# Optimization experiments

Measured on AMD Instinct MI355X. Metric: run time of the kernel, lower is better.

The kernel has to match this reference:

```python
import jax, jax.numpy as jnp
import numpy as np

B, N = 32, 512            # batch, max nodes per graph
F_DIM, M_DIM = 1024, 256  # node feature dim, first hidden dim
N_SEM = 8                 # number of semantic-class experts
XYZ, DIM_E = 3, 8
OUT_SIZE = 2 * XYZ + DIM_E  # 14 (default reg branch)
EPS = 1e-8                # padding value used by out_seq_to_batch


def setup_inputs() -> dict:
    key = jax.random.key(0)
    ks = jax.random.split(key, 12)
    def w(k, shape, fan_in):
        return jax.random.normal(k, shape, jnp.float32) / np.float32(np.sqrt(fan_in))
    return {
        "nodes": jax.random.normal(ks[0], (B, N, F_DIM), jnp.float32),
        "sem": jax.random.randint(ks[1], (B, N), 0, N_SEM, jnp.int32),
        "lengths": jax.random.randint(ks[2], (B,), 64, N + 1, jnp.int32),
        # y expert MLPs (4 layers), stacked over experts
        "W1": w(ks[3], (N_SEM, F_DIM, M_DIM), F_DIM), "b1": jnp.zeros((N_SEM, M_DIM), jnp.float32),
        "W2": w(ks[4], (N_SEM, M_DIM, 64), M_DIM),   "b2": jnp.zeros((N_SEM, 64), jnp.float32),
        "W3": w(ks[5], (N_SEM, 64, 32), 64),         "b3": jnp.zeros((N_SEM, 32), jnp.float32),
        "W4": w(ks[6], (N_SEM, 32, OUT_SIZE), 32),   "b4": jnp.zeros((N_SEM, OUT_SIZE), jnp.float32),
        # rot expert MLPs (2 layers), stacked over experts
        "R1": w(ks[7], (N_SEM, F_DIM, M_DIM), F_DIM), "rb1": jnp.zeros((N_SEM, M_DIM), jnp.float32),
        "R2": w(ks[8], (N_SEM, M_DIM, XYZ), M_DIM),   "rb2": jnp.zeros((N_SEM, XYZ), jnp.float32),
    }


def _prim_mlps(nodes, sem, lengths, W1, b1, W2, b2, W3, b3, W4, b4, R1, rb1, R2, rb2):
    Bn, Nn, Fd = nodes.shape
    x = nodes.reshape(-1, Fd)                       # [T, F], T = B*N tokens
    semf = sem.reshape(-1)                          # [T] expert id per token
    # dense dispatch: run every expert on all tokens, then select per token
    h1 = jax.nn.relu(jnp.einsum('tf,efm->etm', x, W1) + b1[:, None, :])   # [E,T,M]
    h2 = jax.nn.relu(jnp.einsum('etm,emh->eth', h1, W2) + b2[:, None, :]) # [E,T,64]
    h3 = jax.nn.relu(jnp.einsum('eth,ehg->etg', h2, W3) + b3[:, None, :]) # [E,T,32]
    y_all = jnp.einsum('etg,ego->eto', h3, W4) + b4[:, None, :]           # [E,T,OUT]
    r1 = jax.nn.relu(jnp.einsum('tf,efm->etm', x, R1) + rb1[:, None, :])  # [E,T,M]
    rot_all = jnp.einsum('etm,emo->eto', r1, R2) + rb2[:, None, :]        # [E,T,XYZ]
    t = jnp.arange(x.shape[0])
    y = y_all[semf, t]                              # [T, OUT]
    rot = rot_all[semf, t]                          # [T, XYZ]
    out = jnp.concatenate([y, rot], axis=-1).reshape(Bn, Nn, -1)
    # positions beyond each graph's length are filled with eps (out_seq_to_batch)
    mask = (jnp.arange(Nn)[None, :] < lengths[:, None])[:, :, None]
    return jnp.where(mask, out, jnp.float32(EPS))


def reference(nodes, sem, lengths, W1, b1, W2, b2, W3, b3, W4, b4, R1, rb1, R2, rb2):
    return _prim_mlps(nodes, sem, lengths, W1, b1, W2, b2, W3, b3, W4, b4,
                      R1, rb1, R2, rb2)
```

## Files before the change

### kernel.cpp

```cpp
#include <hip/hip_runtime.h>
#include <stdint.h>

#define T_TOK 16384
#define NE 8
#define EPSV 1e-8f
#define MAXC128 136
#define MAXC64  264

#define WS_PERM   0
#define WS_PART   65536
#define WS_OFFS   67584
#define WS_XS     131072
#define WS_WT     (WS_XS + 16512*1024*2)
#define WS_H1     (WS_WT + 8*512*1024*2)
#define WS_W2T    (WS_H1 + 16448*512*2)
#define WS_W3T    (WS_W2T + 8*64*256*2)
#define WS_W4T    (WS_W3T + 8*32*64*2)
#define WS_R2T    (WS_W4T + 8*16*32*2)

typedef __attribute__((ext_vector_type(8))) short bf16x8;
typedef __attribute__((ext_vector_type(4))) float f32x4;

__device__ __forceinline__ unsigned short f2bf(float f) {
    unsigned u = __float_as_uint(f);
    u += 0x7fffu + ((u >> 16) & 1u);
    return (unsigned short)(u >> 16);
}

__device__ __forceinline__ void gl_lds16(const void* g, void* l) {
    __builtin_amdgcn_global_load_lds(
        (const __attribute__((address_space(1))) void*)g,
        (__attribute__((address_space(3))) void*)l,
        16, 0, 0);
}

__device__ __forceinline__ bool chunk_lookup(const int* __restrict__ offs, int c, int csize,
                                             int& e, int& base, int& len) {
    int acc = 0;
#pragma unroll
    for (int i = 0; i < NE; i++) {
        int s = offs[i], t = offs[i + 1];
        int cc = (t - s + csize - 1) / csize;
        if (c < acc + cc) {
            e = i;
            base = s + (c - acc) * csize;
            len = (t - base < csize) ? (t - base) : csize;
            return true;
        }
        acc += cc;
    }
    return false;
}

__global__ __launch_bounds__(256) void k_prep1(const float* __restrict__ W1,
                                               const float* __restrict__ R1,
                                               const float* __restrict__ W2,
                                               const float* __restrict__ W3,
                                               const float* __restrict__ W4,
                                               const float* __restrict__ R2,
                                               const int* __restrict__ sem,
                                               unsigned short* __restrict__ wt,
                                               unsigned short* __restrict__ w2t,
                                               unsigned short* __restrict__ w3t,
                                               unsigned short* __restrict__ w4t,
                                               unsigned short* __restrict__ r2t,
                                               int* __restrict__ ws_i) {
    __shared__ float tile[64][65];
    int id = blockIdx.x, tid = threadIdx.x;
    if (id >= 1024) {
        __shared__ int cnt[NE];
        int hb = id - 1024, lane = tid & 63;
        if (tid < NE) cnt[tid] = 0;
        __syncthreads();
        int s = sem[hb * 256 + tid];
#pragma unroll
        for (int e = 0; e < NE; e++) {
            unsigned long long m = __ballot(s == e);
            if (lane == e) atomicAdd(&cnt[e], (int)__popcll(m));
        }
        __syncthreads();
        if (tid < NE) ws_i[(WS_PART >> 2) + hb * NE + tid] = cnt[tid];
        return;
    }
    int e = id >> 7, rem = id & 127;
    int ny = rem >> 4, kx = rem & 15;
    int k0 = kx * 64, n0 = ny * 64;
    const float* src = (n0 < 256) ? (W1 + (size_t)e * 1024 * 256 + n0)
                                  : (R1 + (size_t)e * 1024 * 256 + (n0 - 256));
    int rr = tid >> 4;
    int cg = (tid & 15) * 4;
#pragma unroll
    for (int p = 0; p < 4; p++) {
        int kk = p * 16 + rr;
        float4 v = *(const float4*)(src + (size_t)(k0 + kk) * 256 + cg);
        tile[kk][cg] = v.x; tile[kk][cg + 1] = v.y; tile[kk][cg + 2] = v.z; tile[kk][cg + 3] = v.w;
    }
    __syncthreads();
    int nn = tid >> 3;
    int k8 = tid & 7;
#pragma unroll
    for (int p = 0; p < 2; p++) {
        int n = p * 32 + nn;
        unsigned w[4];
#pragma unroll
        for (int j = 0; j < 4; j++) {
            float f0 = tile[k8 * 8 + 2 * j][n];
            float f1 = tile[k8 * 8 + 2 * j + 1][n];
            w[j] = (unsigned)f2bf(f0) | ((unsigned)f2bf(f1) << 16);
        }
        *(uint4*)(wt + (size_t)(e * 512 + n0 + n) * 1024 + k0 + k8 * 8) =
            make_uint4(w[0], w[1], w[2], w[3]);
    }
    if (ny == 0) {
        int x = kx;
        for (int j = tid; j < 1024; j += 256) {
            int idx = x * 1024 + j; int k = idx & 255, n = idx >> 8;
            w2t[(size_t)(e * 64 + n) * 256 + k] = f2bf(W2[(size_t)e * 16384 + k * 64 + n]);
        }
        if (tid < 128) {
            int idx = x * 128 + tid; int k = idx & 63, n = idx >> 6;
            w3t[(size_t)(e * 32 + n) * 64 + k] = f2bf(W3[(size_t)e * 2048 + k * 32 + n]);
        }
        if (tid < 32) {
            int idx = x * 32 + tid; int k = idx & 31, n = idx >> 5;
            w4t[(size_t)(e * 16 + n) * 32 + k] = (n < 14) ? f2bf(W4[(size_t)e * 448 + k * 14 + n])
                                                          : (unsigned short)0;
        }
        {
            int idx = x * 256 + tid; int k = idx & 255, n = idx >> 8;
            r2t[(size_t)(e * 16 + n) * 256 + k] = (n < 3) ? f2bf(R2[(size_t)e * 768 + k * 3 + n])
                                                          : (unsigned short)0;
        }
    }
}

__global__ __launch_bounds__(256) void k_scatter(const int* __restrict__ sem,
                                                 const float* __restrict__ nodes,
                                                 int* __restrict__ ws_i,
                                                 unsigned short* __restrict__ xs) {
    __shared__ int parts[512];
    __shared__ int tot[NE], preb[NE], ebase[NE + 1];
    __shared__ int wcnt[4][NE];
    __shared__ int destS[256];
    int b = blockIdx.x, g = b >> 3, j = b & 7;
    int tid = threadIdx.x, wave = tid >> 6, lane = tid & 63;
    parts[tid] = ws_i[(WS_PART >> 2) + tid];
    parts[256 + tid] = ws_i[(WS_PART >> 2) + 256 + tid];
    __syncthreads();
    if (tid < NE) {
        int t = 0, p = 0;
        for (int bb = 0; bb < 64; bb++) {
            int v = parts[bb * NE + tid];
            t += v;
            if (bb < g) p += v;
        }
        tot[tid] = t; preb[tid] = p;
    }
    __syncthreads();
    if (tid == 0) {
        int base = 0;
        for (int e = 0; e < NE; e++) { ebase[e] = base; base += tot[e]; }
        ebase[NE] = base;
        if (b == 0)
            for (int e = 0; e <= NE; e++) ws_i[(WS_OFFS >> 2) + e] = ebase[e];
    }
    int i = g * 256 + tid;
    int s = sem[i];
    int rank = 0;
#pragma unroll
    for (int e = 0; e < NE; e++) {
        unsigned long long m = __ballot(s == e);
        if (s == e) rank = (int)__popcll(m & ((1ull << lane) - 1ull));
        if (lane == e) wcnt[wave][e] = (int)__popcll(m);
    }
    __syncthreads();
    int wpre = 0;
#pragma unroll
    for (int w = 0; w < 4; w++)
        if (w < wave) wpre += wcnt[w][s];
    int dest = ebase[s] + preb[s] + wpre + rank;
    destS[tid] = dest;
    if (j == 0) ws_i[(WS_PERM >> 2) + dest] = i;
    __syncthreads();
#pragma unroll 4
    for (int r = j * 32; r < j * 32 + 32; r++) {
        int tok = g * 256 + r;
        int d = destS[r];
        float4 v = *(const float4*)(nodes + (size_t)tok * 1024 + tid * 4);
        unsigned p0 = (unsigned)f2bf(v.x) | ((unsigned)f2bf(v.y) << 16);
        unsigned p1 = (unsigned)f2bf(v.z) | ((unsigned)f2bf(v.w) << 16);
        *(uint2*)(xs + (size_t)d * 1024 + tid * 4) = make_uint2(p0, p1);
    }
}

__global__ __launch_bounds__(256) void k_gemm(const unsigned short* __restrict__ xs,
                                              const unsigned short* __restrict__ wt,
                                              const float* __restrict__ b1,
                                              const float* __restrict__ rb1,
                                              const int* __restrict__ ws_i,
                                              unsigned short* __restrict__ h1) {
    __shared__ __align__(16) short As[64 * 64];
    __shared__ __align__(16) short Bs[128 * 64];
    int e, base, len;
    if (!chunk_lookup(ws_i + (WS_OFFS >> 2), blockIdx.x, 64, e, base, len)) return;
    int n0 = blockIdx.y * 128;
    int tid = threadIdx.x;
    int wave = tid >> 6, lane = tid & 63;
    int quad = lane >> 4, lr = lane & 15;
    int wn = wave * 32;

    f32x4 acc[4][2];
#pragma unroll
    for (int i = 0; i < 4; i++)
#pragma unroll
        for (int j = 0; j < 2; j++) acc[i][j] = (f32x4){0.f, 0.f, 0.f, 0.f};

    const unsigned short* Ag = xs + (size_t)base * 1024;
    const unsigned short* Bg = wt + (size_t)(e * 512 + n0) * 1024;

    const unsigned short* srcA[2];
    int dstA[2];
#pragma unroll
    for (int i = 0; i < 2; i++) {
        int s = i * 256 + wave * 64 + lane;
        int r = s >> 3, cs = (s & 7) ^ (r & 7);
        srcA[i] = Ag + (size_t)r * 1024 + cs * 8;
        dstA[i] = (i * 256 + wave * 64) * 8;
    }
    const unsigned short* srcB[4];
    int dstB[4];
#pragma unroll
    for (int i = 0; i < 4; i++) {
        int s = i * 256 + wave * 64 + lane;
        int r = s >> 3, cs = (s & 7) ^ (r & 7);
        srcB[i] = Bg + (size_t)r * 1024 + cs * 8;
        dstB[i] = (i * 256 + wave * 64) * 8;
    }

    for (int kb = 0; kb < 16; kb++) {
        __syncthreads();
#pragma unroll
        for (int i = 0; i < 2; i++) gl_lds16(srcA[i] + kb * 64, As + dstA[i]);
#pragma unroll
        for (int i = 0; i < 4; i++) gl_lds16(srcB[i] + kb * 64, Bs + dstB[i]);
        __syncthreads();

        bf16x8 af[2][4], bfr[2][2];
#pragma unroll
        for (int im = 0; im < 4; im++) {
            int r = im * 16 + lr;
#pragma unroll
            for (int kh = 0; kh < 2; kh++) {
                int q = kh * 4 + quad;
                af[kh][im] = *(const bf16x8*)(As + (r * 8 + (q ^ (r & 7))) * 8);
            }
        }
#pragma unroll
        for (int in = 0; in < 2; in++) {
            int r = wn + in * 16 + lr;
#pragma unroll
            for (int kh = 0; kh < 2; kh++) {
                int q = kh * 4 + quad;
                bfr[kh][in] = *(const bf16x8*)(Bs + (r * 8 + (q ^ (r & 7))) * 8);
            }
        }
#pragma unroll
        for (int kh = 0; kh < 2; kh++)
#pragma unroll
            for (int im = 0; im < 4; im++)
#pragma unroll
                for (int in = 0; in < 2; in++)
                    acc[im][in] = __builtin_amdgcn_mfma_f32_16x16x32_bf16(af[kh][im], bfr[kh][in], acc[im][in], 0, 0, 0);
    }

#pragma unroll
    for (int in = 0; in < 2; in++) {
        int gcol = n0 + wn + in * 16 + lr;
        float bias = (gcol < 256) ? b1[e * 256 + gcol] : rb1[e * 256 + gcol - 256];
#pragma unroll
        for (int im = 0; im < 4; im++) {
#pragma unroll
            for (int v = 0; v < 4; v++) {
                int r = im * 16 + quad * 4 + v;
                if (r < len) {
                    float val = fmaxf(acc[im][in][v] + bias, 0.f);
                    h1[(size_t)(base + r) * 512 + gcol] = f2bf(val);
                }
            }
        }
    }
}

__global__ __launch_bounds__(256) void k_tail(const unsigned short* __restrict__ h1,
                                              const int* __restrict__ ws_i,
                                              const unsigned short* __restrict__ w2t,
                                              const unsigned short* __restrict__ w3t,
                                              const unsigned short* __restrict__ w4t,
                                              const unsigned short* __restrict__ r2t,
                                              const float* __restrict__ b2,
                                              const float* __restrict__ b3,
                                              const float* __restrict__ b4,
                                              const float* __restrict__ rb2,
                                              const int* __restrict__ lengths,
                                              float* __restrict__ out) {
    __shared__ __align__(16) unsigned short h2s[4][16][64];
    __shared__ __align__(16) unsigned short h3s[4][16][32];

    int e, base, len;
    if (!chunk_lookup(ws_i + (WS_OFFS >> 2), blockIdx.x, 64, e, base, len)) return;
    int tid = threadIdx.x, wave = tid >> 6, lane = tid & 63;
    int quad = lane >> 4, lr = lane & 15;
    int m0 = wave * 16;

    const unsigned short* Ap = h1 + (size_t)(base + m0) * 512;

    f32x4 acc2[4];
#pragma unroll
    for (int t = 0; t < 4; t++) {
        float bb = b2[e * 64 + t * 16 + lr];
        acc2[t] = (f32x4){bb, bb, bb, bb};
    }
    f32x4 accr;
    { float bb = (lr < 3) ? rb2[e * 3 + lr] : 0.f; accr = (f32x4){bb, bb, bb, bb}; }

    const unsigned short* W2e = w2t + (size_t)e * 64 * 256;
    const unsigned short* R2e = r2t + (size_t)e * 16 * 256;
#pragma unroll
    for (int kk = 0; kk < 8; kk++) {
        int k0 = kk * 32;
        bf16x8 a = *(const bf16x8*)(Ap + lr * 512 + k0 + quad * 8);
#pragma unroll
        for (int t = 0; t < 4; t++) {
            bf16x8 b = *(const bf16x8*)(W2e + (t * 16 + lr) * 256 + k0 + quad * 8);
            acc2[t] = __builtin_amdgcn_mfma_f32_16x16x32_bf16(a, b, acc2[t], 0, 0, 0);
        }
        bf16x8 ar = *(const bf16x8*)(Ap + lr * 512 + 256 + k0 + quad * 8);
        bf16x8 br = *(const bf16x8*)(R2e + lr * 256 + k0 + quad * 8);
        accr = __builtin_amdgcn_mfma_f32_16x16x32_bf16(ar, br, accr, 0, 0, 0);
    }
#pragma unroll
    for (int t = 0; t < 4; t++)
#pragma unroll
        for (int v = 0; v < 4; v++)
            h2s[wave][quad * 4 + v][t * 16 + lr] = f2bf(fmaxf(acc2[t][v], 0.f));

    f32x4 acc3[2];
#pragma unroll
    for (int t = 0; t < 2; t++) {
        float bb = b3[e * 32 + t * 16 + lr];
        acc3[t] = (f32x4){bb, bb, bb, bb};
    }
    const unsigned short* W3e = w3t + (size_t)e * 32 * 64;
#pragma unroll
    for (int kk = 0; kk < 2; kk++) {
        int k0 = kk * 32;
        bf16x8 a = *(const bf16x8*)(&h2s[wave][lr][k0 + quad * 8]);
#pragma unroll
        for (int t = 0; t < 2; t++) {
            bf16x8 b = *(const bf16x8*)(W3e + (t * 16 + lr) * 64 + k0 + quad * 8);
            acc3[t] = __builtin_amdgcn_mfma_f32_16x16x32_bf16(a, b, acc3[t], 0, 0, 0);
        }
    }
#pragma unroll
    for (int t = 0; t < 2; t++)
#pragma unroll
        for (int v = 0; v < 4; v++)
            h3s[wave][quad * 4 + v][t * 16 + lr] = f2bf(fmaxf(acc3[t][v], 0.f));

    f32x4 acc4;
    { float bb = (lr < 14) ? b4[e * 14 + lr] : 0.f; acc4 = (f32x4){bb, bb, bb, bb}; }
    {
        bf16x8 a = *(const bf16x8*)(&h3s[wave][lr][quad * 8]);
        bf16x8 b = *(const bf16x8*)(w4t + ((size_t)e * 16 + lr) * 32 + quad * 8);
        acc4 = __builtin_amdgcn_mfma_f32_16x16x32_bf16(a, b, acc4, 0, 0, 0);
    }

    const int* perm = ws_i + (WS_PERM >> 2);
#pragma unroll
    for (int v = 0; v < 4; v++) {
        int t = m0 + quad * 4 + v;
        if (t < len) {
            int token = perm[base + t];
            int bi = token >> 9, ni = token & 511;
            int valid = ni < lengths[bi];
            if (lr < 14) out[(size_t)token * 17 + lr] = valid ? acc4[v] : EPSV;
            if (lr < 3)  out[(size_t)token * 17 + 14 + lr] = valid ? accr[v] : EPSV;
        }
    }
}

extern "C" void kernel_launch(void* const* d_in, const int* in_sizes, int n_in,
                              void* d_out, int out_size, void* d_ws, size_t ws_size,
                              hipStream_t stream) {
    (void)in_sizes; (void)n_in; (void)out_size; (void)ws_size;
    const float* nodes   = (const float*)d_in[0];
    const int*   sem     = (const int*)d_in[1];
    const int*   lengths = (const int*)d_in[2];
    const float* W1 = (const float*)d_in[3];
    const float* b1 = (const float*)d_in[4];
    const float* W2 = (const float*)d_in[5];
    const float* b2 = (const float*)d_in[6];
    const float* W3 = (const float*)d_in[7];
    const float* b3 = (const float*)d_in[8];
    const float* W4 = (const float*)d_in[9];
    const float* b4 = (const float*)d_in[10];
    const float* R1  = (const float*)d_in[11];
    const float* rb1 = (const float*)d_in[12];
    const float* R2  = (const float*)d_in[13];
    const float* rb2 = (const float*)d_in[14];
    float* out = (float*)d_out;

    char* ws = (char*)d_ws;
    int* ws_i = (int*)ws;
    unsigned short* xs  = (unsigned short*)(ws + WS_XS);
    unsigned short* wt  = (unsigned short*)(ws + WS_WT);
    unsigned short* h1  = (unsigned short*)(ws + WS_H1);
    unsigned short* w2t = (unsigned short*)(ws + WS_W2T);
    unsigned short* w3t = (unsigned short*)(ws + WS_W3T);
    unsigned short* w4t = (unsigned short*)(ws + WS_W4T);
    unsigned short* r2t = (unsigned short*)(ws + WS_R2T);

    hipLaunchKernelGGL(k_prep1, dim3(1088), dim3(256), 0, stream,
                       W1, R1, W2, W3, W4, R2, sem, wt, w2t, w3t, w4t, r2t, ws_i);
    hipLaunchKernelGGL(k_scatter, dim3(512), dim3(256), 0, stream, sem, nodes, ws_i, xs);
    hipLaunchKernelGGL(k_gemm, dim3(MAXC64, 4), dim3(256), 0, stream,
                       (const unsigned short*)xs, (const unsigned short*)wt, b1, rb1,
                       (const int*)ws_i, h1);
    hipLaunchKernelGGL(k_tail, dim3(MAXC64), dim3(256), 0, stream,
                       (const unsigned short*)h1, (const int*)ws_i,
                       (const unsigned short*)w2t, (const unsigned short*)w3t,
                       (const unsigned short*)w4t, (const unsigned short*)r2t,
                       b2, b3, b4, rb2, lengths, out);
}
```

Baseline: 204.2 us.

## Double-buffer LDS tiles in expert GEMM to overlap global loads with MFMA

The first-layer expert GEMM now keeps two LDS buffers for the A and B tiles. It issues the global-to-LDS loads for the next k-block before computing the current one, using explicit vmcnt waits and s_barrier in place of the two __syncthreads per iteration. The aim is to hide global memory latency behind MFMA work. LDS use doubles to 48KB per block, which may lower occupancy, and correctness depends on the hand-counted vmcnt value.

```diff
diff --git a/kernel.cpp b/kernel.cpp
--- a/kernel.cpp
+++ b/kernel.cpp
@@ -199,8 +199,8 @@
                                               const float* __restrict__ rb1,
                                               const int* __restrict__ ws_i,
                                               unsigned short* __restrict__ h1) {
-    __shared__ __align__(16) short As[64 * 64];
-    __shared__ __align__(16) short Bs[128 * 64];
+    __shared__ __align__(16) short As[2][64 * 64];
+    __shared__ __align__(16) short Bs[2][128 * 64];
     int e, base, len;
     if (!chunk_lookup(ws_i + (WS_OFFS >> 2), blockIdx.x, 64, e, base, len)) return;
     int n0 = blockIdx.y * 128;
@@ -237,14 +237,28 @@
         dstB[i] = (i * 256 + wave * 64) * 8;
     }
 
+#pragma unroll
+    for (int i = 0; i < 2; i++) gl_lds16(srcA[i], &As[0][dstA[i]]);
+#pragma unroll
+    for (int i = 0; i < 4; i++) gl_lds16(srcB[i], &Bs[0][dstB[i]]);
+
     for (int kb = 0; kb < 16; kb++) {
-        __syncthreads();
-#pragma unroll
-        for (int i = 0; i < 2; i++) gl_lds16(srcA[i] + kb * 64, As + dstA[i]);
-#pragma unroll
-        for (int i = 0; i < 4; i++) gl_lds16(srcB[i] + kb * 64, Bs + dstB[i]);
-        __syncthreads();
-
+        int cur = kb & 1;
+        if (kb < 15) {
+            int nxt = cur ^ 1;
+#pragma unroll
+            for (int i = 0; i < 2; i++) gl_lds16(srcA[i] + (kb + 1) * 64, &As[nxt][dstA[i]]);
+#pragma unroll
+            for (int i = 0; i < 4; i++) gl_lds16(srcB[i] + (kb + 1) * 64, &Bs[nxt][dstB[i]]);
+            asm volatile("s_waitcnt vmcnt(6)" ::: "memory");
+        } else {
+            asm volatile("s_waitcnt vmcnt(0)" ::: "memory");
+        }
+        __builtin_amdgcn_sched_barrier(0);
+        __builtin_amdgcn_s_barrier();
+
+        const short* Ab = As[cur];
+        const short* Bb = Bs[cur];
         bf16x8 af[2][4], bfr[2][2];
 #pragma unroll
         for (int im = 0; im < 4; im++) {
@@ -252,7 +266,7 @@
 #pragma unroll
             for (int kh = 0; kh < 2; kh++) {
                 int q = kh * 4 + quad;
-                af[kh][im] = *(const bf16x8*)(As + (r * 8 + (q ^ (r & 7))) * 8);
+                af[kh][im] = *(const bf16x8*)(Ab + (r * 8 + (q ^ (r & 7))) * 8);
             }
         }
 #pragma unroll
@@ -261,7 +275,7 @@
 #pragma unroll
             for (int kh = 0; kh < 2; kh++) {
                 int q = kh * 4 + quad;
-                bfr[kh][in] = *(const bf16x8*)(Bs + (r * 8 + (q ^ (r & 7))) * 8);
+                bfr[kh][in] = *(const bf16x8*)(Bb + (r * 8 + (q ^ (r & 7))) * 8);
             }
         }
 #pragma unroll
@@ -271,6 +285,11 @@
 #pragma unroll
                 for (int in = 0; in < 2; in++)
                     acc[im][in] = __builtin_amdgcn_mfma_f32_16x16x32_bf16(af[kh][im], bfr[kh][in], acc[im][in], 0, 0, 0);
+
+        if (kb < 15) {
+            __builtin_amdgcn_sched_barrier(0);
+            __builtin_amdgcn_s_barrier();
+        }
     }
 
 #pragma unroll
```

New measurement: 194.2 us. -4.9%, faster.

## Load GEMM fragments directly from global memory with register double buffering

Applied to the files above, without the earlier changes.

The expert GEMM stops staging A and B tiles through LDS with per-step barriers. Each lane now reads its MFMA fragments straight from global memory into two register sets, alternating loads and MFMAs to hide latency. The grid is flattened to 1D and block ids are remapped so neighbouring workgroups land on different XCDs. This removes LDS traffic and syncthreads, but every wave re-reads the A tile from global/L2 instead of sharing it, and register pressure goes up.

```diff
diff --git a/kernel.cpp b/kernel.cpp
--- a/kernel.cpp
+++ b/kernel.cpp
@@ -193,17 +193,42 @@
     }
 }
 
+#define LOAD_STEP(af, bfr, kb) do {                                              \
+    _Pragma("unroll")                                                            \
+    for (int im_ = 0; im_ < 4; im_++) {                                          \
+        af[0][im_] = pA[im_][0][(kb) * 8];                                       \
+        af[1][im_] = pA[im_][1][(kb) * 8];                                       \
+    }                                                                            \
+    _Pragma("unroll")                                                            \
+    for (int in_ = 0; in_ < 2; in_++) {                                          \
+        bfr[0][in_] = pB[in_][0][(kb) * 8];                                      \
+        bfr[1][in_] = pB[in_][1][(kb) * 8];                                      \
+    }                                                                            \
+} while (0)
+
+#define MFMA_STEP(af, bfr) do {                                                  \
+    _Pragma("unroll")                                                            \
+    for (int kh_ = 0; kh_ < 2; kh_++)                                            \
+    _Pragma("unroll")                                                            \
+    for (int im_ = 0; im_ < 4; im_++)                                            \
+    _Pragma("unroll")                                                            \
+    for (int in_ = 0; in_ < 2; in_++)                                            \
+        acc[im_][in_] = __builtin_amdgcn_mfma_f32_16x16x32_bf16(                 \
+            af[kh_][im_], bfr[kh_][in_], acc[im_][in_], 0, 0, 0);                \
+} while (0)
+
 __global__ __launch_bounds__(256) void k_gemm(const unsigned short* __restrict__ xs,
                                               const unsigned short* __restrict__ wt,
                                               const float* __restrict__ b1,
                                               const float* __restrict__ rb1,
                                               const int* __restrict__ ws_i,
                                               unsigned short* __restrict__ h1) {
-    __shared__ __align__(16) short As[64 * 64];
-    __shared__ __align__(16) short Bs[128 * 64];
+    int bid = blockIdx.x;
+    int wgid = (bid & 7) * ((MAXC64 * 4) / 8) + (bid >> 3);
+    int c = wgid >> 2, nblk = wgid & 3;
     int e, base, len;
-    if (!chunk_lookup(ws_i + (WS_OFFS >> 2), blockIdx.x, 64, e, base, len)) return;
-    int n0 = blockIdx.y * 128;
+    if (!chunk_lookup(ws_i + (WS_OFFS >> 2), c, 64, e, base, len)) return;
+    int n0 = nblk * 128;
     int tid = threadIdx.x;
     int wave = tid >> 6, lane = tid & 63;
     int quad = lane >> 4, lr = lane & 15;
@@ -218,60 +243,30 @@
     const unsigned short* Ag = xs + (size_t)base * 1024;
     const unsigned short* Bg = wt + (size_t)(e * 512 + n0) * 1024;
 
-    const unsigned short* srcA[2];
-    int dstA[2];
-#pragma unroll
-    for (int i = 0; i < 2; i++) {
-        int s = i * 256 + wave * 64 + lane;
-        int r = s >> 3, cs = (s & 7) ^ (r & 7);
-        srcA[i] = Ag + (size_t)r * 1024 + cs * 8;
-        dstA[i] = (i * 256 + wave * 64) * 8;
-    }
-    const unsigned short* srcB[4];
-    int dstB[4];
-#pragma unroll
-    for (int i = 0; i < 4; i++) {
-        int s = i * 256 + wave * 64 + lane;
-        int r = s >> 3, cs = (s & 7) ^ (r & 7);
-        srcB[i] = Bg + (size_t)r * 1024 + cs * 8;
-        dstB[i] = (i * 256 + wave * 64) * 8;
-    }
-
-    for (int kb = 0; kb < 16; kb++) {
-        __syncthreads();
-#pragma unroll
-        for (int i = 0; i < 2; i++) gl_lds16(srcA[i] + kb * 64, As + dstA[i]);
-#pragma unroll
-        for (int i = 0; i < 4; i++) gl_lds16(srcB[i] + kb * 64, Bs + dstB[i]);
-        __syncthreads();
-
-        bf16x8 af[2][4], bfr[2][2];
-#pragma unroll
-        for (int im = 0; im < 4; im++) {
-            int r = im * 16 + lr;
-#pragma unroll
-            for (int kh = 0; kh < 2; kh++) {
-                int q = kh * 4 + quad;
-                af[kh][im] = *(const bf16x8*)(As + (r * 8 + (q ^ (r & 7))) * 8);
-            }
-        }
-#pragma unroll
-        for (int in = 0; in < 2; in++) {
-            int r = wn + in * 16 + lr;
-#pragma unroll
-            for (int kh = 0; kh < 2; kh++) {
-                int q = kh * 4 + quad;
-                bfr[kh][in] = *(const bf16x8*)(Bs + (r * 8 + (q ^ (r & 7))) * 8);
-            }
-        }
+    const bf16x8* pA[4][2];
+#pragma unroll
+    for (int im = 0; im < 4; im++)
 #pragma unroll
         for (int kh = 0; kh < 2; kh++)
-#pragma unroll
-            for (int im = 0; im < 4; im++)
-#pragma unroll
-                for (int in = 0; in < 2; in++)
-                    acc[im][in] = __builtin_amdgcn_mfma_f32_16x16x32_bf16(af[kh][im], bfr[kh][in], acc[im][in], 0, 0, 0);
-    }
+            pA[im][kh] = (const bf16x8*)(Ag + (size_t)(im * 16 + lr) * 1024 + (kh * 4 + quad) * 8);
+    const bf16x8* pB[2][2];
+#pragma unroll
+    for (int in = 0; in < 2; in++)
+#pragma unroll
+        for (int kh = 0; kh < 2; kh++)
+            pB[in][kh] = (const bf16x8*)(Bg + (size_t)(wn + in * 16 + lr) * 1024 + (kh * 4 + quad) * 8);
+
+    bf16x8 afA[2][4], bfA[2][2], afB[2][4], bfB[2][2];
+    LOAD_STEP(afA, bfA, 0);
+    LOAD_STEP(afB, bfB, 1);
+    for (int kb = 0; kb < 14; kb += 2) {
+        MFMA_STEP(afA, bfA);
+        LOAD_STEP(afA, bfA, kb + 2);
+        MFMA_STEP(afB, bfB);
+        LOAD_STEP(afB, bfB, kb + 3);
+    }
+    MFMA_STEP(afA, bfA);
+    MFMA_STEP(afB, bfB);
 
 #pragma unroll
     for (int in = 0; in < 2; in++) {
@@ -423,7 +418,7 @@
     hipLaunchKernelGGL(k_prep1, dim3(1088), dim3(256), 0, stream,
                        W1, R1, W2, W3, W4, R2, sem, wt, w2t, w3t, w4t, r2t, ws_i);
     hipLaunchKernelGGL(k_scatter, dim3(512), dim3(256), 0, stream, sem, nodes, ws_i, xs);
-    hipLaunchKernelGGL(k_gemm, dim3(MAXC64, 4), dim3(256), 0, stream,
+    hipLaunchKernelGGL(k_gemm, dim3(MAXC64 * 4), dim3(256), 0, stream,
                        (const unsigned short*)xs, (const unsigned short*)wt, b1, rb1,
                        (const int*)ws_i, h1);
     hipLaunchKernelGGL(k_tail, dim3(MAXC64), dim3(256), 0, stream,
```

New measurement: 275.2 us. 1.35x slower.
